# Optimization experiments

Hardware: AMD Instinct MI355X
Metric: run time of the kernel (lower is better)

The kernel has to match this reference:

```python
import jax, jax.numpy as jnp
import numpy as np

P = 512        # n_predicates
C = 65536      # n_constants
L = 1          # max_rule_length (only runnable config of original code)


def setup_inputs() -> dict:
    key = jax.random.key(0)
    k1, k2 = jax.random.split(key)
    initial_facts = jax.random.uniform(k1, (P, C), dtype=jnp.float32)
    rule_weights = jax.random.normal(k2, (P, L, P), dtype=jnp.float32)
    return {"initial_facts": initial_facts, "rule_weights": rule_weights, "n_iterations": 3}


def reference(initial_facts, rule_weights, n_iterations):
    # F.softmax(rule[step], dim=0) on the 1-D vector rule_weights[r, 0, :]
    # == softmax over the last axis of rule_weights[:, 0, :].
    # Stacking apply_rule over all rules r is exactly A @ facts.
    A = jax.nn.softmax(rule_weights[:, 0, :], axis=-1)  # [P, P]
    facts = initial_facts                                # [P, C]
    for _ in range(n_iterations):
        derived = A @ facts                              # [P, C] (rule r -> row r)
        facts = jnp.maximum(facts, derived.max(axis=0))  # broadcast [C] over [P, C]
    return facts
```

## Files before the change

kernel.cpp:

```cpp
#include <hip/hip_runtime.h>
#include <hip/hip_bf16.h>
#include <cstdint>


typedef __attribute__((ext_vector_type(8))) short bf16x8;
typedef __attribute__((ext_vector_type(8))) unsigned short u16x8;
typedef __attribute__((ext_vector_type(16))) float f32x16;
typedef unsigned short ushort_t;
typedef unsigned int uint32;

#define PDIM 512
#define CDIM 65536
#define NT   64

__device__ __forceinline__ ushort_t f2bf(float x) {
    uint32 u = __float_as_uint(x);
    return (ushort_t)((u + 0x7fffu + ((u >> 16) & 1u)) >> 16);
}
__device__ __forceinline__ float bf2f(uint32 bits) { return __uint_as_float(bits << 16); }

__device__ __forceinline__ bf16x8 pkmax8(bf16x8 v, ushort_t mu) {
    u16x8 a = __builtin_bit_cast(u16x8, v);
    const u16x8 mb = {mu, mu, mu, mu, mu, mu, mu, mu};
    a = __builtin_elementwise_max(a, mb);
    return __builtin_bit_cast(bf16x8, a);
}

__global__ __launch_bounds__(64) void softmax_pack(const float* __restrict__ rw,
                                                   ushort_t* __restrict__ Apk) {
    const int r  = blockIdx.x;
    const int ln = threadIdx.x;
    const float* row = rw + r * PDIM;
    float4 x0 = *(const float4*)(row + ln * 8);
    float4 x1 = *(const float4*)(row + ln * 8 + 4);
    float v[8] = {x0.x, x0.y, x0.z, x0.w, x1.x, x1.y, x1.z, x1.w};

    float mx = -1e30f;
    #pragma unroll
    for (int i = 0; i < 8; ++i) mx = fmaxf(mx, v[i]);
    #pragma unroll
    for (int d = 1; d < 64; d <<= 1) mx = fmaxf(mx, __shfl_xor(mx, d, 64));
    float s = 0.f;
    #pragma unroll
    for (int i = 0; i < 8; ++i) { v[i] = __expf(v[i] - mx); s += v[i]; }
    #pragma unroll
    for (int d = 1; d < 64; d <<= 1) s += __shfl_xor(s, d, 64);
    const float inv = 1.f / s;

    ushort_t o[8];
    #pragma unroll
    for (int i = 0; i < 8; ++i) o[i] = f2bf(v[i] * inv);
    const int idx16 = ((ln >> 1) * 16 + (r >> 5)) * 64 + ((ln & 1) << 5) + (r & 31);
    *(int4*)(Apk + idx16 * 8) = *(const int4*)o;
}

__global__ __launch_bounds__(256, 2) void ilp_kernel(
        const float* __restrict__ facts,
        const ushort_t* __restrict__ Apk,
        const int* __restrict__ n_iter_p,
        float* __restrict__ out) {
    __shared__ ushort_t ft[NT * PDIM];
    __shared__ float wred[2][4][NT];
    __shared__ float mfin[NT];

    const int tid  = threadIdx.x;
    const int wave = tid >> 6;
    const int lane = tid & 63;
    const int l31  = lane & 31;
    const int half = lane >> 5;
    const int c0   = blockIdx.x * NT;

    int n_iter = *n_iter_p;
    n_iter = n_iter < 0 ? 0 : (n_iter > 8 ? 8 : n_iter);

    {
        const int ch  = (tid & 31) * 2;
        const int pb  = tid >> 5;
        const int key = ((ch >> 1) & 7) << 3;
        #pragma unroll 4
        for (int s = 0; s < 8; ++s) {
            const int p0 = s * 64 + pb * 8;
            ushort_t ga[8], gb[8];
            #pragma unroll
            for (int i = 0; i < 8; ++i) {
                const float2 v = *(const float2*)(facts + (p0 + i) * CDIM + c0 + ch);
                ga[i] = f2bf(v.x);
                gb[i] = f2bf(v.y);
            }
            *(int4*)(&ft[ch * PDIM + (p0 ^ key)])       = *(const int4*)ga;
            *(int4*)(&ft[(ch + 1) * PDIM + (p0 ^ key)]) = *(const int4*)gb;
        }
    }
    __syncthreads();

    const ushort_t* abase = Apk + (wave * 256 + half * 32 + l31) * 8;
    int cbase2[2], ckey2[2];
    #pragma unroll
    for (int ct2 = 0; ct2 < 2; ++ct2) {
        const int c = ct2 * 32 + l31;
        cbase2[ct2] = c * PDIM;
        ckey2[ct2]  = ((c >> 1) & 7) << 3;
    }

    ushort_t ml[2] = {0, 0};
    float    mf[2] = {0.f, 0.f};

    bf16x8 aF[2][4], bR[2][2];
    {
        #pragma unroll
        for (int rt2 = 0; rt2 < 4; ++rt2) aF[0][rt2] = *(const bf16x8*)(abase + rt2 * 512);
        const int gh = half * 8;
        #pragma unroll
        for (int ct2 = 0; ct2 < 2; ++ct2)
            bR[0][ct2] = *(const bf16x8*)(&ft[cbase2[ct2] + (gh ^ ckey2[ct2])]);
    }

    #pragma unroll 1
    for (int it = 0; it < n_iter; ++it) {
        f32x16 acc[4][2];
        #pragma unroll
        for (int rt2 = 0; rt2 < 4; ++rt2)
            #pragma unroll
            for (int ct2 = 0; ct2 < 2; ++ct2)
                #pragma unroll
                for (int e = 0; e < 16; ++e) acc[rt2][ct2][e] = 0.f;

        #pragma unroll 2
        for (int kt2 = 0; kt2 < 32; ++kt2) {
            const int cur = kt2 & 1, nxt = cur ^ 1;
            const int ktn = (kt2 + 1) & 31;
            {
                const ushort_t* ap = abase + ktn * 8192;
                #pragma unroll
                for (int rt2 = 0; rt2 < 4; ++rt2)
                    aF[nxt][rt2] = *(const bf16x8*)(ap + rt2 * 512);
            }
            {
                const int gh = (ktn * 2 + half) * 8;
                #pragma unroll
                for (int ct2 = 0; ct2 < 2; ++ct2)
                    bR[nxt][ct2] = *(const bf16x8*)(&ft[cbase2[ct2] + (gh ^ ckey2[ct2])]);
            }
            bf16x8 bC[2];
            #pragma unroll
            for (int ct2 = 0; ct2 < 2; ++ct2) bC[ct2] = pkmax8(bR[cur][ct2], ml[ct2]);

            __builtin_amdgcn_s_setprio(1);
            #pragma unroll
            for (int rt2 = 0; rt2 < 4; ++rt2)
                #pragma unroll
                for (int ct2 = 0; ct2 < 2; ++ct2)
                    acc[rt2][ct2] = __builtin_amdgcn_mfma_f32_32x32x16_bf16(
                        aF[cur][rt2], bC[ct2], acc[rt2][ct2], 0, 0, 0);
            __builtin_amdgcn_s_setprio(0);
        }

        float mx[2];
        #pragma unroll
        for (int ct2 = 0; ct2 < 2; ++ct2) {
            float m0 = -1e30f;
            #pragma unroll
            for (int rt2 = 0; rt2 < 4; ++rt2)
                #pragma unroll
                for (int e = 0; e < 16; ++e) m0 = fmaxf(m0, acc[rt2][ct2][e]);
            m0 = fmaxf(m0, __shfl_xor(m0, 32, 64));
            mx[ct2] = m0;
        }
        const int buf = it & 1;
        if (half == 0) {
            #pragma unroll
            for (int ct2 = 0; ct2 < 2; ++ct2) wred[buf][wave][ct2 * 32 + l31] = mx[ct2];
        }
        __syncthreads();
        #pragma unroll
        for (int ct2 = 0; ct2 < 2; ++ct2) {
            const int c = ct2 * 32 + l31;
            const float m = fmaxf(fmaxf(wred[buf][0][c], wred[buf][1][c]),
                                  fmaxf(wred[buf][2][c], wred[buf][3][c]));
            mf[ct2] = fmaxf(mf[ct2], m);
            ml[ct2] = f2bf(mf[ct2]);
        }
    }

    if (wave == 0 && half == 0) {
        #pragma unroll
        for (int ct2 = 0; ct2 < 2; ++ct2) mfin[ct2 * 32 + l31] = mf[ct2];
    }
    __syncthreads();

    {
        const int ch  = (tid & 31) * 2;
        const int pb  = tid >> 5;
        const int key = ((ch >> 1) & 7) << 3;
        const float ma = mfin[ch];
        const float mb = mfin[ch + 1];
        for (int s = 0; s < 8; ++s) {
            const int p0 = s * 64 + pb * 8;
            ushort_t ga[8], gb[8];
            *(int4*)ga = *(const int4*)(&ft[ch * PDIM + (p0 ^ key)]);
            *(int4*)gb = *(const int4*)(&ft[(ch + 1) * PDIM + (p0 ^ key)]);
            #pragma unroll
            for (int i = 0; i < 8; ++i) {
                float2 v;
                v.x = fmaxf(bf2f(ga[i]), ma);
                v.y = fmaxf(bf2f(gb[i]), mb);
                *(float2*)(out + (p0 + i) * CDIM + c0 + ch) = v;
            }
        }
    }
}

extern "C" void kernel_launch(void* const* d_in, const int* in_sizes, int n_in,
                              void* d_out, int out_size, void* d_ws, size_t ws_size,
                              hipStream_t stream) {
    const float* facts    = (const float*)d_in[0];
    const float* rw       = (const float*)d_in[1];
    const int*   n_iter_p = (const int*)d_in[2];
    float* out = (float*)d_out;

    ushort_t* Apk = (ushort_t*)d_ws;

    softmax_pack<<<PDIM, 64, 0, stream>>>(rw, Apk);
    ilp_kernel<<<CDIM / NT, 256, 0, stream>>>(facts, Apk, n_iter_p, out);
}
```

Measured before the change: 303.0 us.

## Use 8 waves per block with k-group LDS layout and fewer accumulators

Raises the block to 512 threads (8 waves), so each wave computes two 32-row tiles instead of four, roughly halving accumulator registers and allowing higher occupancy. The LDS facts tile moves from a swizzled column-major layout to a k-group-major layout, which makes B-fragment reads contiguous. Global loads and stores become one float per thread, coalesced across 64 columns. The cost is less work per wave to hide latency, more waves in the reduction barrier, and narrower global accesses.

```diff
diff --git a/kernel.cpp b/kernel.cpp
--- a/kernel.cpp
+++ b/kernel.cpp
@@ -12,6 +12,7 @@
 #define PDIM 512
 #define CDIM 65536
 #define NT   64
+#define WAVES 8
 
 __device__ __forceinline__ ushort_t f2bf(float x) {
     uint32 u = __float_as_uint(x);
@@ -54,13 +55,13 @@
     *(int4*)(Apk + idx16 * 8) = *(const int4*)o;
 }
 
-__global__ __launch_bounds__(256, 2) void ilp_kernel(
+__global__ __launch_bounds__(512, 4) void ilp_kernel(
         const float* __restrict__ facts,
         const ushort_t* __restrict__ Apk,
         const int* __restrict__ n_iter_p,
         float* __restrict__ out) {
-    __shared__ ushort_t ft[NT * PDIM];
-    __shared__ float wred[2][4][NT];
+    __shared__ ushort_t ft[64 * NT * 8];
+    __shared__ float wred[2][WAVES][NT];
     __shared__ float mfin[NT];
 
     const int tid  = threadIdx.x;
@@ -74,52 +75,37 @@
     n_iter = n_iter < 0 ? 0 : (n_iter > 8 ? 8 : n_iter);
 
     {
-        const int ch  = (tid & 31) * 2;
-        const int pb  = tid >> 5;
-        const int key = ((ch >> 1) & 7) << 3;
-        #pragma unroll 4
+        const int c = tid & 63;
+        #pragma unroll 2
         for (int s = 0; s < 8; ++s) {
-            const int p0 = s * 64 + pb * 8;
-            ushort_t ga[8], gb[8];
-            #pragma unroll
-            for (int i = 0; i < 8; ++i) {
-                const float2 v = *(const float2*)(facts + (p0 + i) * CDIM + c0 + ch);
-                ga[i] = f2bf(v.x);
-                gb[i] = f2bf(v.y);
-            }
-            *(int4*)(&ft[ch * PDIM + (p0 ^ key)])       = *(const int4*)ga;
-            *(int4*)(&ft[(ch + 1) * PDIM + (p0 ^ key)]) = *(const int4*)gb;
-        }
-    }
+            const int g = wave * 8 + s;
+            ushort_t gb[8];
+            #pragma unroll
+            for (int i = 0; i < 8; ++i)
+                gb[i] = f2bf(facts[(g * 8 + i) * CDIM + c0 + c]);
+            *(int4*)(&ft[(g * 64 + c) * 8]) = *(const int4*)gb;
+        }
+    }
+
+    const ushort_t* abase = Apk + (wave * 128 + half * 32 + l31) * 8;
+    bf16x8 aF[2][2], bR[2][2];
+    aF[0][0] = *(const bf16x8*)(abase);
+    aF[0][1] = *(const bf16x8*)(abase + 512);
+
     __syncthreads();
 
-    const ushort_t* abase = Apk + (wave * 256 + half * 32 + l31) * 8;
-    int cbase2[2], ckey2[2];
-    #pragma unroll
-    for (int ct2 = 0; ct2 < 2; ++ct2) {
-        const int c = ct2 * 32 + l31;
-        cbase2[ct2] = c * PDIM;
-        ckey2[ct2]  = ((c >> 1) & 7) << 3;
-    }
+    const int bbase = (half * 64 + l31) * 8;
+    bR[0][0] = *(const bf16x8*)(&ft[bbase]);
+    bR[0][1] = *(const bf16x8*)(&ft[bbase + 256]);
 
     ushort_t ml[2] = {0, 0};
     float    mf[2] = {0.f, 0.f};
 
-    bf16x8 aF[2][4], bR[2][2];
-    {
-        #pragma unroll
-        for (int rt2 = 0; rt2 < 4; ++rt2) aF[0][rt2] = *(const bf16x8*)(abase + rt2 * 512);
-        const int gh = half * 8;
-        #pragma unroll
-        for (int ct2 = 0; ct2 < 2; ++ct2)
-            bR[0][ct2] = *(const bf16x8*)(&ft[cbase2[ct2] + (gh ^ ckey2[ct2])]);
-    }
-
     #pragma unroll 1
     for (int it = 0; it < n_iter; ++it) {
-        f32x16 acc[4][2];
+        f32x16 acc[2][2];
         #pragma unroll
-        for (int rt2 = 0; rt2 < 4; ++rt2)
+        for (int rt2 = 0; rt2 < 2; ++rt2)
             #pragma unroll
             for (int ct2 = 0; ct2 < 2; ++ct2)
                 #pragma unroll
@@ -131,27 +117,23 @@
             const int ktn = (kt2 + 1) & 31;
             {
                 const ushort_t* ap = abase + ktn * 8192;
-                #pragma unroll
-                for (int rt2 = 0; rt2 < 4; ++rt2)
-                    aF[nxt][rt2] = *(const bf16x8*)(ap + rt2 * 512);
+                aF[nxt][0] = *(const bf16x8*)(ap);
+                aF[nxt][1] = *(const bf16x8*)(ap + 512);
             }
             {
-                const int gh = (ktn * 2 + half) * 8;
-                #pragma unroll
-                for (int ct2 = 0; ct2 < 2; ++ct2)
-                    bR[nxt][ct2] = *(const bf16x8*)(&ft[cbase2[ct2] + (gh ^ ckey2[ct2])]);
+                const int bo = bbase + ktn * 1024;
+                bR[nxt][0] = *(const bf16x8*)(&ft[bo]);
+                bR[nxt][1] = *(const bf16x8*)(&ft[bo + 256]);
             }
-            bf16x8 bC[2];
-            #pragma unroll
-            for (int ct2 = 0; ct2 < 2; ++ct2) bC[ct2] = pkmax8(bR[cur][ct2], ml[ct2]);
-
             __builtin_amdgcn_s_setprio(1);
             #pragma unroll
-            for (int rt2 = 0; rt2 < 4; ++rt2)
-                #pragma unroll
-                for (int ct2 = 0; ct2 < 2; ++ct2)
-                    acc[rt2][ct2] = __builtin_amdgcn_mfma_f32_32x32x16_bf16(
-                        aF[cur][rt2], bC[ct2], acc[rt2][ct2], 0, 0, 0);
+            for (int ct2 = 0; ct2 < 2; ++ct2) {
+                const bf16x8 bC = pkmax8(bR[cur][ct2], ml[ct2]);
+                acc[0][ct2] = __builtin_amdgcn_mfma_f32_32x32x16_bf16(
+                    aF[cur][0], bC, acc[0][ct2], 0, 0, 0);
+                acc[1][ct2] = __builtin_amdgcn_mfma_f32_32x32x16_bf16(
+                    aF[cur][1], bC, acc[1][ct2], 0, 0, 0);
+            }
             __builtin_amdgcn_s_setprio(0);
         }
 
@@ -160,7 +142,7 @@
         for (int ct2 = 0; ct2 < 2; ++ct2) {
             float m0 = -1e30f;
             #pragma unroll
-            for (int rt2 = 0; rt2 < 4; ++rt2)
+            for (int rt2 = 0; rt2 < 2; ++rt2)
                 #pragma unroll
                 for (int e = 0; e < 16; ++e) m0 = fmaxf(m0, acc[rt2][ct2][e]);
             m0 = fmaxf(m0, __shfl_xor(m0, 32, 64));
@@ -175,37 +157,31 @@
         #pragma unroll
         for (int ct2 = 0; ct2 < 2; ++ct2) {
             const int c = ct2 * 32 + l31;
-            const float m = fmaxf(fmaxf(wred[buf][0][c], wred[buf][1][c]),
-                                  fmaxf(wred[buf][2][c], wred[buf][3][c]));
+            float m = wred[buf][0][c];
+            #pragma unroll
+            for (int w = 1; w < WAVES; ++w) m = fmaxf(m, wred[buf][w][c]);
             mf[ct2] = fmaxf(mf[ct2], m);
             ml[ct2] = f2bf(mf[ct2]);
         }
     }
 
     if (wave == 0 && half == 0) {
-        #pragma unroll
-        for (int ct2 = 0; ct2 < 2; ++ct2) mfin[ct2 * 32 + l31] = mf[ct2];
+        mfin[l31]      = mf[0];
+        mfin[32 + l31] = mf[1];
     }
     __syncthreads();
 
     {
-        const int ch  = (tid & 31) * 2;
-        const int pb  = tid >> 5;
-        const int key = ((ch >> 1) & 7) << 3;
-        const float ma = mfin[ch];
-        const float mb = mfin[ch + 1];
+        const int c = tid & 63;
+        const float m = mfin[c];
+        #pragma unroll 2
         for (int s = 0; s < 8; ++s) {
-            const int p0 = s * 64 + pb * 8;
-            ushort_t ga[8], gb[8];
-            *(int4*)ga = *(const int4*)(&ft[ch * PDIM + (p0 ^ key)]);
-            *(int4*)gb = *(const int4*)(&ft[(ch + 1) * PDIM + (p0 ^ key)]);
-            #pragma unroll
-            for (int i = 0; i < 8; ++i) {
-                float2 v;
-                v.x = fmaxf(bf2f(ga[i]), ma);
-                v.y = fmaxf(bf2f(gb[i]), mb);
-                *(float2*)(out + (p0 + i) * CDIM + c0 + ch) = v;
-            }
+            const int g = wave * 8 + s;
+            ushort_t gb[8];
+            *(int4*)gb = *(const int4*)(&ft[(g * 64 + c) * 8]);
+            #pragma unroll
+            for (int i = 0; i < 8; ++i)
+                out[(g * 8 + i) * CDIM + c0 + c] = fmaxf(bf2f(gb[i]), m);
         }
     }
 }
@@ -221,5 +197,5 @@
     ushort_t* Apk = (ushort_t*)d_ws;
 
     softmax_pack<<<PDIM, 64, 0, stream>>>(rw, Apk);
-    ilp_kernel<<<CDIM / NT, 256, 0, stream>>>(facts, Apk, n_iter_p, out);
-}
+    ilp_kernel<<<CDIM / NT, 512, 0, stream>>>(facts, Apk, n_iter_p, out);
+}
```

Result: no change. 307.5 us (+1.5%).
